# Kernel tuning notes

Measured on AMD Instinct MI355X. Metric: run time of the kernel, lower is better.

Reference implementation:

```python
import jax, jax.numpy as jnp
import numpy as np

B, CIN, COUT, H, W, KK = 1, 32, 64, 181, 360, 4
NNZ_PER, NNZ_PER1 = 9, 4


def _make_psi(rng, K, H, W, nnz_per):
    # Sparse DISCO basis in COO form for longitude 0 (shift-invariant in lon).
    E = K * H * nnz_per
    seg = np.repeat(np.arange(K * H, dtype=np.int32), nnz_per)  # k*H + ho
    ho = seg % H
    dlat = rng.integers(-1, 2, size=E).astype(np.int32)
    hi = np.clip(ho + dlat, 0, H - 1).astype(np.int32)
    wi = (rng.integers(-1, 2, size=E).astype(np.int32)) % W
    vals = (rng.normal(size=E) * 0.2).astype(np.float32)
    return seg, hi, wi, vals


def setup_inputs() -> dict:
    rng = np.random.default_rng(0)
    key = jax.random.key(0)
    ks = jax.random.split(key, 5)
    x = jax.random.normal(ks[0], (B, CIN, H, W), dtype=jnp.float32)
    # spherical quadrature weights: sin(colatitude) * cell area
    theta = np.linspace(0.0, np.pi, H)
    qw = (np.sin(theta) * (np.pi / (H - 1)) * (2.0 * np.pi / W)).astype(np.float32)
    qw = np.maximum(qw, 1e-8).reshape(H, 1)
    seg, hi, wi, vals = _make_psi(rng, KK, H, W, NNZ_PER)
    seg1, hi1, wi1, vals1 = _make_psi(rng, 1, H, W, NNZ_PER1)
    w_depth = jax.random.normal(ks[1], (CIN, KK), dtype=jnp.float32) / np.sqrt(KK)
    w_point = jax.random.normal(ks[2], (COUT, CIN), dtype=jnp.float32) / np.sqrt(CIN)
    bias = jax.random.normal(ks[3], (COUT,), dtype=jnp.float32) * 0.02
    return {
        "x": x,
        "quad_w": jnp.asarray(qw),
        "vals": jnp.asarray(vals),
        "seg": jnp.asarray(seg),
        "hi": jnp.asarray(hi),
        "wi": jnp.asarray(wi),
        "w_depth": w_depth,
        "vals1": jnp.asarray(vals1),
        "seg1": jnp.asarray(seg1),
        "hi1": jnp.asarray(hi1),
        "wi1": jnp.asarray(wi1),
        "w_point": w_point,
        "bias": bias,
        "K": KK,
    }


def _disco_contract(x, vals, seg, hi, wi, K):
    # x: [B,C,H,W]; COO psi at lon 0; out[b,c,k,ho,wo] =
    #   sum_{e: seg[e]==k*H+ho} vals[e] * x[b,c,hi[e],(wi[e]+wo) mod W]
    Bq, C, Hq, Wq = x.shape
    rows = x[:, :, hi, :]                                        # [B,C,E,W]
    col = (wi[:, None] + jnp.arange(Wq, dtype=wi.dtype)[None, :]) % Wq  # [E,W]
    rolled = jnp.take_along_axis(rows, col[None, None, :, :], axis=3)   # [B,C,E,W]
    weighted = rolled * vals[None, None, :, None]
    out = jax.ops.segment_sum(weighted.transpose(2, 0, 1, 3), seg,
                              num_segments=K * Hq)               # [K*H,B,C,W]
    return out.reshape(K, Hq, Bq, C, Wq).transpose(2, 3, 0, 1, 4)  # [B,C,K,H,W]


def reference(x, quad_w, vals, seg, hi, wi, w_depth, vals1, seg1, hi1, wi1,
              w_point, bias, K):
    # depthwise DISCO conv (groups=C_in, no bias)
    xq = x * quad_w                                   # quadrature weighting
    xd = _disco_contract(xq, vals, seg, hi, wi, K)    # [B,C,K,H,W]
    y = jnp.einsum("ck,bckhw->bchw", w_depth, xd)     # per-channel K mix
    # pointwise DISCO conv (kernel_shape=1) = CLinear
    yq = y * quad_w
    z = _disco_contract(yq, vals1, seg1, hi1, wi1, 1)[:, :, 0]  # [B,C,H,W]
    out = jnp.einsum("oc,bchw->bohw", w_point, z) + bias[None, :, None, None]
    return out
```

## Files before the change

### kernel.cpp

```cpp
#include <hip/hip_runtime.h>


#define H_    181
#define W_    360
#define CIN_  32
#define COUT_ 64
#define K_    4
#define NNZ_  9
#define NNZ1_ 4
#define HW_   (H_*W_)
#define NT_   (NNZ1_*K_*NNZ_)
#define CSZ_  (CIN_*25)

__global__ __launch_bounds__(256) void coef_build(
    const float* __restrict__ quad_w, const float* __restrict__ vals,
    const int* __restrict__ hi, const int* __restrict__ wi,
    const float* __restrict__ w_depth, const float* __restrict__ vals1,
    const int* __restrict__ hi1, const int* __restrict__ wi1,
    float* __restrict__ Cg)
{
    const int h   = blockIdx.x;
    const int tid = threadIdx.x;

    __shared__ float Tval[NT_];
    __shared__ int   Tbin[NT_];
    __shared__ float S[K_][25];

    if (tid < NT_) {
        const int a   = tid / 36;
        const int rem = tid - a * 36;
        const int k   = rem / 9;
        const int j   = rem - k * 9;
        const int e1  = h * NNZ1_ + a;
        const int m   = hi1[e1];
        const int w1  = wi1[e1];
        const int d1  = (w1 == 1) ? 1 : ((w1 == 0) ? 0 : -1);
        const int e   = (k * H_ + m) * NNZ_ + j;
        const int r   = hi[e];
        const int ww  = wi[e];
        const int d   = (ww == 1) ? 1 : ((ww == 0) ? 0 : -1);
        Tval[tid] = vals1[e1] * quad_w[m] * vals[e] * quad_w[r];
        Tbin[tid] = (r - h + 2) * 5 + (d1 + d + 2);
    }
    __syncthreads();

    if (tid < K_ * 25) {
        const int k   = tid / 25;
        const int bin = tid - k * 25;
        float s = 0.f;
        #pragma unroll
        for (int a = 0; a < NNZ1_; ++a)
            #pragma unroll
            for (int j = 0; j < NNZ_; ++j) {
                const int t2 = a * 36 + k * 9 + j;
                if (Tbin[t2] == bin) s += Tval[t2];
            }
        S[k][bin] = s;
    }
    __syncthreads();

    for (int i = tid; i < CSZ_; i += 256) {
        const int cc = i / 25, bin = i - cc * 25;
        float acc = 0.f;
        #pragma unroll
        for (int k = 0; k < K_; ++k) acc += w_depth[cc * K_ + k] * S[k][bin];
        Cg[h * CSZ_ + i] = acc;
    }
}

__global__ __launch_bounds__(512) void sepconv_main(
    const float* __restrict__ x, const float* __restrict__ Cg,
    const float* __restrict__ w_point, const float* __restrict__ bias,
    float* __restrict__ out)
{
    const int bx = blockIdx.x;
    const int h  = (bx & 7) * 23 + (bx >> 3);
    if (h >= H_) return;
    const int seg = blockIdx.y;
    const int w0  = seg * 64;
    const int pxn = (seg == 5) ? 40 : 64;
    const int gn  = pxn >> 2;
    const int tid = threadIdx.x;

    __shared__ __attribute__((aligned(16))) float C[CIN_][25];
    __shared__ float zs[64][33];

    const int g = tid & 15;
    const int c = tid >> 4;
    const bool act = (g < gn);

    int rowoff[5];
    #pragma unroll
    for (int rb = 0; rb < 5; ++rb) {
        int r = h - 2 + rb;
        r = (r < 0) ? 0 : ((r > H_ - 1) ? H_ - 1 : r);
        rowoff[rb] = r * W_;
    }

    const int bw = w0 + g * 4;
    const int cA = (bw + W_ - 4) % W_;
    const int cB = bw;
    const int cC = (bw + 4) % W_;

    float4 L[15];
    if (act) {
        const float* xc = x + c * HW_;
        #pragma unroll
        for (int rb = 0; rb < 5; ++rb) {
            const float* xr = xc + rowoff[rb];
            L[rb * 3 + 0] = *(const float4*)(xr + cA);
            L[rb * 3 + 1] = *(const float4*)(xr + cB);
            L[rb * 3 + 2] = *(const float4*)(xr + cC);
        }
    }

    if (tid < CSZ_ / 2)
        ((float2*)&C[0][0])[tid] =
            ((const float2*)(Cg + h * CSZ_))[tid];
    __syncthreads();

    if (act) {
        const float* Cc = &C[c][0];
        float a0 = 0.f, a1 = 0.f, a2 = 0.f, a3 = 0.f;
        #pragma unroll
        for (int rb = 0; rb < 5; ++rb) {
            const float4 vA = L[rb * 3 + 0];
            const float4 vB = L[rb * 3 + 1];
            const float4 vC = L[rb * 3 + 2];
            const float k0 = Cc[rb * 5 + 0], k1 = Cc[rb * 5 + 1],
                        k2 = Cc[rb * 5 + 2], k3 = Cc[rb * 5 + 3],
                        k4 = Cc[rb * 5 + 4];
            a0 += k0 * vA.z + k1 * vA.w + k2 * vB.x + k3 * vB.y + k4 * vB.z;
            a1 += k0 * vA.w + k1 * vB.x + k2 * vB.y + k3 * vB.z + k4 * vB.w;
            a2 += k0 * vB.x + k1 * vB.y + k2 * vB.z + k3 * vB.w + k4 * vC.x;
            a3 += k0 * vB.y + k1 * vB.z + k2 * vB.w + k3 * vC.x + k4 * vC.y;
        }
        const int p = g * 4;
        zs[p + 0][c] = a0;
        zs[p + 1][c] = a1;
        zs[p + 2][c] = a2;
        zs[p + 3][c] = a3;
    }
    __syncthreads();

    const int j  = tid & 63;
    const int oh = tid >> 6;
    if (j < pxn) {
        float zr[CIN_];
        #pragma unroll
        for (int cc = 0; cc < CIN_; ++cc) zr[cc] = zs[j][cc];

        const float* wp = w_point + oh * 8 * CIN_;
        float* op = out + oh * 8 * HW_ + h * W_ + w0 + j;
        #pragma unroll
        for (int oo = 0; oo < 8; ++oo) {
            float acc = bias[oh * 8 + oo];
            #pragma unroll
            for (int cc = 0; cc < CIN_; ++cc)
                acc += wp[oo * CIN_ + cc] * zr[cc];
            op[oo * HW_] = acc;
        }
    }
}

extern "C" void kernel_launch(void* const* d_in, const int* in_sizes, int n_in,
                              void* d_out, int out_size, void* d_ws, size_t ws_size,
                              hipStream_t stream) {
    const float* x       = (const float*)d_in[0];
    const float* quad_w  = (const float*)d_in[1];
    const float* vals    = (const float*)d_in[2];
    const int*   hi      = (const int*)d_in[4];
    const int*   wi      = (const int*)d_in[5];
    const float* w_depth = (const float*)d_in[6];
    const float* vals1   = (const float*)d_in[7];
    const int*   hi1     = (const int*)d_in[9];
    const int*   wi1     = (const int*)d_in[10];
    const float* w_point = (const float*)d_in[11];
    const float* bias    = (const float*)d_in[12];

    float* Cg = (float*)d_ws;

    coef_build<<<dim3(181), 256, 0, stream>>>(
        quad_w, vals, hi, wi, w_depth, vals1, hi1, wi1, Cg);
    sepconv_main<<<dim3(184, 6), 512, 0, stream>>>(
        x, Cg, w_point, bias, (float*)d_out);
}
```

Before: 115.9 us.

## Split fused stencil+pointwise kernel into separate stencil and pointwise kernels

After: 114.0 us. No clear change (-1.7%).

```diff
diff --git a/kernel.cpp b/kernel.cpp
--- a/kernel.cpp
+++ b/kernel.cpp
@@ -10,7 +10,9 @@
 #define NNZ1_ 4
 #define HW_   (H_*W_)
 #define NT_   (NNZ1_*K_*NNZ_)
-#define CSZ_  (CIN_*25)
+#define CROW_ 32
+#define CSZH_ (CIN_*CROW_)
+#define ZOFF_ ((size_t)1 << 20)
 
 __global__ __launch_bounds__(256) void coef_build(
     const float* __restrict__ quad_w, const float* __restrict__ vals,
@@ -59,107 +61,102 @@
     }
     __syncthreads();
 
-    for (int i = tid; i < CSZ_; i += 256) {
+    for (int i = tid; i < CIN_ * 25; i += 256) {
         const int cc = i / 25, bin = i - cc * 25;
         float acc = 0.f;
         #pragma unroll
         for (int k = 0; k < K_; ++k) acc += w_depth[cc * K_ + k] * S[k][bin];
-        Cg[h * CSZ_ + i] = acc;
+        Cg[h * CSZH_ + cc * CROW_ + bin] = acc;
     }
 }
 
-__global__ __launch_bounds__(512) void sepconv_main(
+__global__ __launch_bounds__(256) void stencil_z(
     const float* __restrict__ x, const float* __restrict__ Cg,
-    const float* __restrict__ w_point, const float* __restrict__ bias,
-    float* __restrict__ out)
+    float* __restrict__ z)
 {
-    const int bx = blockIdx.x;
-    const int h  = (bx & 7) * 23 + (bx >> 3);
-    if (h >= H_) return;
-    const int seg = blockIdx.y;
-    const int w0  = seg * 64;
-    const int pxn = (seg == 5) ? 40 : 64;
-    const int gn  = pxn >> 2;
-    const int tid = threadIdx.x;
+    const int nwg  = (int)gridDim.x;
+    const int orig = (int)blockIdx.x;
+    const int q = nwg >> 3, r = nwg & 7;
+    const int xcd = orig & 7, off = orig >> 3;
+    const int wg  = (xcd < r ? xcd * (q + 1)
+                             : r * (q + 1) + (xcd - r) * q) + off;
 
-    __shared__ __attribute__((aligned(16))) float C[CIN_][25];
-    __shared__ float zs[64][33];
-
-    const int g = tid & 15;
-    const int c = tid >> 4;
-    const bool act = (g < gn);
+    const int lin = wg * 256 + (int)threadIdx.x;
+    if (lin >= CIN_ * H_ * 90) return;
+    const int c   = lin / (H_ * 90);
+    const int rem = lin - c * (H_ * 90);
+    const int h   = rem / 90;
+    const int g   = rem - h * 90;
 
     int rowoff[5];
     #pragma unroll
     for (int rb = 0; rb < 5; ++rb) {
-        int r = h - 2 + rb;
-        r = (r < 0) ? 0 : ((r > H_ - 1) ? H_ - 1 : r);
-        rowoff[rb] = r * W_;
+        int rr = h - 2 + rb;
+        rr = (rr < 0) ? 0 : ((rr > H_ - 1) ? H_ - 1 : rr);
+        rowoff[rb] = rr * W_;
     }
-
-    const int bw = w0 + g * 4;
+    const int bw = g * 4;
     const int cA = (bw + W_ - 4) % W_;
     const int cB = bw;
     const int cC = (bw + 4) % W_;
 
+    const float* xc = x + c * HW_;
     float4 L[15];
-    if (act) {
-        const float* xc = x + c * HW_;
-        #pragma unroll
-        for (int rb = 0; rb < 5; ++rb) {
-            const float* xr = xc + rowoff[rb];
-            L[rb * 3 + 0] = *(const float4*)(xr + cA);
-            L[rb * 3 + 1] = *(const float4*)(xr + cB);
-            L[rb * 3 + 2] = *(const float4*)(xr + cC);
-        }
+    #pragma unroll
+    for (int rb = 0; rb < 5; ++rb) {
+        const float* xr = xc + rowoff[rb];
+        L[rb * 3 + 0] = *(const float4*)(xr + cA);
+        L[rb * 3 + 1] = *(const float4*)(xr + cB);
+        L[rb * 3 + 2] = *(const float4*)(xr + cC);
     }
 
-    if (tid < CSZ_ / 2)
-        ((float2*)&C[0][0])[tid] =
-            ((const float2*)(Cg + h * CSZ_))[tid];
-    __syncthreads();
+    const float* Cc = Cg + h * CSZH_ + c * CROW_;
+    float k[28];
+    #pragma unroll
+    for (int i = 0; i < 7; ++i)
+        ((float4*)k)[i] = ((const float4*)Cc)[i];
 
-    if (act) {
-        const float* Cc = &C[c][0];
-        float a0 = 0.f, a1 = 0.f, a2 = 0.f, a3 = 0.f;
+    float a0 = 0.f, a1 = 0.f, a2 = 0.f, a3 = 0.f;
+    #pragma unroll
+    for (int rb = 0; rb < 5; ++rb) {
+        const float4 vA = L[rb * 3 + 0];
+        const float4 vB = L[rb * 3 + 1];
+        const float4 vC = L[rb * 3 + 2];
+        const float k0 = k[rb * 5 + 0], k1 = k[rb * 5 + 1],
+                    k2 = k[rb * 5 + 2], k3 = k[rb * 5 + 3],
+                    k4 = k[rb * 5 + 4];
+        a0 += k0 * vA.z + k1 * vA.w + k2 * vB.x + k3 * vB.y + k4 * vB.z;
+        a1 += k0 * vA.w + k1 * vB.x + k2 * vB.y + k3 * vB.z + k4 * vB.w;
+        a2 += k0 * vB.x + k1 * vB.y + k2 * vB.z + k3 * vB.w + k4 * vC.x;
+        a3 += k0 * vB.y + k1 * vB.z + k2 * vB.w + k3 * vC.x + k4 * vC.y;
+    }
+    *(float4*)(z + c * HW_ + h * W_ + bw) = make_float4(a0, a1, a2, a3);
+}
+
+__global__ __launch_bounds__(512) void pointwise(
+    const float* __restrict__ z, const float* __restrict__ w_point,
+    const float* __restrict__ bias, float* __restrict__ out)
+{
+    const int tid = (int)threadIdx.x;
+    const int oq  = __builtin_amdgcn_readfirstlane(tid >> 7);
+    const int p   = tid & 127;
+    const int px  = (int)blockIdx.x * 128 + p;
+    if (px >= HW_) return;
+
+    float zr[CIN_];
+    #pragma unroll
+    for (int cc = 0; cc < CIN_; ++cc) zr[cc] = z[cc * HW_ + px];
+
+    const float* wp = w_point + oq * 16 * CIN_;
+    const float* bq = bias + oq * 16;
+    float* op = out + oq * 16 * HW_ + px;
+    #pragma unroll 4
+    for (int o = 0; o < 16; ++o) {
+        float acc = bq[o];
         #pragma unroll
-        for (int rb = 0; rb < 5; ++rb) {
-            const float4 vA = L[rb * 3 + 0];
-            const float4 vB = L[rb * 3 + 1];
-            const float4 vC = L[rb * 3 + 2];
-            const float k0 = Cc[rb * 5 + 0], k1 = Cc[rb * 5 + 1],
-                        k2 = Cc[rb * 5 + 2], k3 = Cc[rb * 5 + 3],
-                        k4 = Cc[rb * 5 + 4];
-            a0 += k0 * vA.z + k1 * vA.w + k2 * vB.x + k3 * vB.y + k4 * vB.z;
-            a1 += k0 * vA.w + k1 * vB.x + k2 * vB.y + k3 * vB.z + k4 * vB.w;
-            a2 += k0 * vB.x + k1 * vB.y + k2 * vB.z + k3 * vB.w + k4 * vC.x;
-            a3 += k0 * vB.y + k1 * vB.z + k2 * vB.w + k3 * vC.x + k4 * vC.y;
-        }
-        const int p = g * 4;
-        zs[p + 0][c] = a0;
-        zs[p + 1][c] = a1;
-        zs[p + 2][c] = a2;
-        zs[p + 3][c] = a3;
-    }
-    __syncthreads();
-
-    const int j  = tid & 63;
-    const int oh = tid >> 6;
-    if (j < pxn) {
-        float zr[CIN_];
-        #pragma unroll
-        for (int cc = 0; cc < CIN_; ++cc) zr[cc] = zs[j][cc];
-
-        const float* wp = w_point + oh * 8 * CIN_;
-        float* op = out + oh * 8 * HW_ + h * W_ + w0 + j;
-        #pragma unroll
-        for (int oo = 0; oo < 8; ++oo) {
-            float acc = bias[oh * 8 + oo];
-            #pragma unroll
-            for (int cc = 0; cc < CIN_; ++cc)
-                acc += wp[oo * CIN_ + cc] * zr[cc];
-            op[oo * HW_] = acc;
-        }
+        for (int cc = 0; cc < CIN_; ++cc)
+            acc += wp[o * CIN_ + cc] * zr[cc];
+        op[o * HW_] = acc;
     }
 }
 
@@ -179,9 +176,12 @@
     const float* bias    = (const float*)d_in[12];
 
     float* Cg = (float*)d_ws;
+    float* z  = (float*)((char*)d_ws + ZOFF_);
 
     coef_build<<<dim3(181), 256, 0, stream>>>(
         quad_w, vals, hi, wi, w_depth, vals1, hi1, wi1, Cg);
-    sepconv_main<<<dim3(184, 6), 512, 0, stream>>>(
-        x, Cg, w_point, bias, (float*)d_out);
+    stencil_z<<<dim3((CIN_ * H_ * 90 + 255) / 256), 256, 0, stream>>>(
+        x, Cg, z);
+    pointwise<<<dim3((HW_ + 127) / 128), 512, 0, stream>>>(
+        z, w_point, bias, (float*)d_out);
 }
```
